# Performance work log

Hardware: AMD Instinct MI355X
Metric: run time of the kernel (lower is better)

The kernel has to match this reference:

```python
import jax, jax.numpy as jnp
import numpy as np

V, E, H, B, S = 32000, 1024, 1024, 64, 128


def setup_inputs() -> dict:
    key = jax.random.key(0)
    ks = jax.random.split(key, 16)
    s = 0.02
    return {
        "input_seq": jax.random.randint(ks[0], (B, 1), 0, V),
        "hidden": jax.random.normal(ks[1], (1, B, H), jnp.float32),
        "cell": jax.random.normal(ks[2], (1, B, H), jnp.float32),
        "encoder_outputs": jax.random.normal(ks[3], (B, S, H), jnp.float32),
        "emb": jax.random.normal(ks[4], (V, E), jnp.float32) * s,
        "Wa_w": jax.random.normal(ks[5], (H, H), jnp.float32) * s,
        "Wa_b": jnp.zeros((H,), jnp.float32),
        "Ua_w": jax.random.normal(ks[6], (H, H), jnp.float32) * s,
        "Ua_b": jnp.zeros((H,), jnp.float32),
        "Va_w": jax.random.normal(ks[7], (1, H), jnp.float32) * s,
        "Va_b": jnp.zeros((1,), jnp.float32),
        "W_ih": jax.random.normal(ks[8], (4 * H, E + H), jnp.float32) * s,
        "W_hh": jax.random.normal(ks[9], (4 * H, H), jnp.float32) * s,
        "b_ih": jnp.zeros((4 * H,), jnp.float32),
        "b_hh": jnp.zeros((4 * H,), jnp.float32),
        "out_w": jax.random.normal(ks[10], (V, H), jnp.float32) * s,
        "out_b": jnp.zeros((V,), jnp.float32),
    }


def reference(input_seq, hidden, cell, encoder_outputs, emb, Wa_w, Wa_b, Ua_w, Ua_b,
              Va_w, Va_b, W_ih, W_hh, b_ih, b_hh, out_w, out_b):
    # embedding lookup (dropout p=0 -> identity): [B,1,E]
    embedded = emb[input_seq]
    # query = last layer hidden: [B,1,H]
    query = hidden[-1][:, None, :]
    # Bahdanau additive attention
    q_proj = query @ Wa_w.T + Wa_b                       # [B,1,H]
    k_proj = encoder_outputs @ Ua_w.T + Ua_b             # [B,S,H]
    scores = jnp.tanh(q_proj + k_proj) @ Va_w.T + Va_b   # [B,S,1]
    scores = scores[..., 0][:, None, :]                  # [B,1,S]
    weights = jax.nn.softmax(scores, axis=-1)            # [B,1,S]
    context = jnp.einsum('bqs,bsh->bqh', weights, encoder_outputs)  # [B,1,H]
    # LSTM single step on concat(embedded, context)
    x = jnp.concatenate([embedded, context], axis=2)[:, 0, :]  # [B,E+H]
    h0, c0 = hidden[0], cell[0]
    gates = x @ W_ih.T + b_ih + h0 @ W_hh.T + b_hh       # [B,4H]
    i, f, g, o = jnp.split(gates, 4, axis=-1)
    c1 = jax.nn.sigmoid(f) * c0 + jax.nn.sigmoid(i) * jnp.tanh(g)
    h1 = jax.nn.sigmoid(o) * jnp.tanh(c1)
    output = h1[:, None, :]                              # [B,1,H]
    logits = output @ out_w.T + out_b                    # [B,1,V]
    return logits, h1[None], c1[None], weights
```

## Files before the change

### kernel.cpp

```cpp
#include <hip/hip_runtime.h>
#include <hip/hip_bf16.h>

using short8 = __attribute__((ext_vector_type(8))) short;
using f32x4  = __attribute__((ext_vector_type(4))) float;

__device__ inline unsigned pk2(float lo, float hi) {
    __hip_bfloat162 h = __float22bfloat162_rn(float2{lo, hi});
    return *reinterpret_cast<unsigned*>(&h);
}
__device__ inline short8 cvt8(float4 a, float4 b) {
    union { unsigned u[4]; short8 s; } r;
    r.u[0] = pk2(a.x, a.y); r.u[1] = pk2(a.z, a.w);
    r.u[2] = pk2(b.x, b.y); r.u[3] = pk2(b.z, b.w);
    return r.s;
}
__device__ inline float ftanh(float x) {
    float e = __expf(2.f * x);
    return 1.f - 2.f / (e + 1.f);
}
__device__ inline void gload16(const void* g, void* lds) {
    __builtin_amdgcn_global_load_lds(
        (const __attribute__((address_space(1))) unsigned int*)g,
        (__attribute__((address_space(3))) unsigned int*)lds, 16, 0, 0);
}
__device__ inline short f2b(float f) {
    unsigned u = __float_as_uint(f);
    return (short)((u + 0x7FFFu + ((u >> 16) & 1u)) >> 16);
}

__global__ void k_init(const int* __restrict__ idx, const float* __restrict__ emb,
                       const float* __restrict__ h0, float* __restrict__ xcat,
                       float4* __restrict__ wsz) {
    int i = blockIdx.x * blockDim.x + threadIdx.x;
    if (i < 18432) {
        float4 z = {0.f, 0.f, 0.f, 0.f};
        wsz[i] = z;
    } else if (i < 67584) {
        int j = i - 18432;
        int b = j / 768, q = j - b * 768;
        if (q < 256)
            ((float4*)(xcat + (size_t)b * 3072))[q] =
                ((const float4*)(emb + (size_t)idx[b] * 1024))[q];
        else if (q >= 512)
            ((float4*)(xcat + (size_t)b * 3072))[q] =
                ((const float4*)(h0 + (size_t)b * 1024))[q - 512];
    }
}

__global__ void k_cvt_swz(const float* __restrict__ enc, const float* __restrict__ Ua,
                          short* __restrict__ dst) {
    int i = blockIdx.x * blockDim.x + threadIdx.x;
    if (i >= 9216 * 128) return;
    int row = i >> 7, gi = i & 127;
    int seg = gi >> 3, g = gi & 7;
    const float* src = (row < 8192) ? enc + ((size_t)row << 10)
                                    : Ua + ((size_t)(row - 8192) << 10);
    const float* p = src + (seg << 6) + ((g ^ (row & 7)) << 3);
    float4 v0 = *(const float4*)p;
    float4 v1 = *(const float4*)(p + 4);
    *(short8*)&dst[(size_t)i << 3] = cvt8(v0, v1);
}

__global__ __launch_bounds__(512) void k_attn2(
    const short* __restrict__ Abf, const short* __restrict__ Bbf,
    const float* __restrict__ Uab, const float* __restrict__ Wab,
    const float* __restrict__ qp, const float* __restrict__ Va,
    float* __restrict__ scores) {
    __shared__ short As[2][256 * 64];
    __shared__ short Bs[2][128 * 64];
    const int t = threadIdx.x;
    const int l = t & 63, w = t >> 6;
    const int wm = w >> 1, wn = w & 1;
    const int lr = l & 15, lg = l >> 4;
    const int n0 = blockIdx.x * 128;
    const int r0 = blockIdx.y * 256;

    f32x4 acc[4][4];
#pragma unroll
    for (int i = 0; i < 4; ++i)
#pragma unroll
        for (int j = 0; j < 4; ++j) { f32x4 z = {0.f, 0.f, 0.f, 0.f}; acc[i][j] = z; }

    auto STAGE = [&](int buf, int seg) {
#pragma unroll
        for (int i = 0; i < 4; ++i) {
            int base = i * 512 + w * 64;
            int s = base + l;
            gload16(Abf + (((size_t)r0 + (s >> 3)) << 10) + (seg << 6) + ((s & 7) << 3),
                    (void*)&As[buf][base * 8]);
            if (i < 2)
                gload16(Bbf + (((size_t)8192 + n0 + (s >> 3)) << 10) + (seg << 6) + ((s & 7) << 3),
                        (void*)&Bs[buf][base * 8]);
        }
    };

    STAGE(0, 0);
    __syncthreads();

    for (int seg = 0; seg < 16; ++seg) {
        const int cur = seg & 1;
        if (seg < 15) STAGE(cur ^ 1, seg + 1);
#pragma unroll
        for (int kh = 0; kh < 2; ++kh) {
            short8 a[4], b[4];
#pragma unroll
            for (int i = 0; i < 4; ++i) {
                int ra = wm * 64 + i * 16 + lr;
                a[i] = *(const short8*)&As[cur][ra * 64 + (((kh * 4 + lg) ^ (ra & 7)) << 3)];
                int rb = wn * 64 + i * 16 + lr;
                b[i] = *(const short8*)&Bs[cur][rb * 64 + (((kh * 4 + lg) ^ (rb & 7)) << 3)];
            }
#pragma unroll
            for (int i = 0; i < 4; ++i)
#pragma unroll
                for (int j = 0; j < 4; ++j)
                    acc[i][j] = __builtin_amdgcn_mfma_f32_16x16x32_bf16(a[i], b[j], acc[i][j], 0, 0, 0);
        }
        __syncthreads();
    }

    float va[4], ub[4];
#pragma unroll
    for (int j = 0; j < 4; ++j) {
        int h = n0 + wn * 64 + j * 16 + lr;
        va[j] = Va[h];
        ub[j] = Uab[h] + Wab[h];
    }
#pragma unroll
    for (int i = 0; i < 4; ++i)
#pragma unroll
        for (int r = 0; r < 4; ++r) {
            int row = r0 + wm * 64 + i * 16 + lg * 4 + r;
            const float* qpb = qp + (size_t)(row >> 7) * 1024;
            float s = 0.f;
#pragma unroll
            for (int j = 0; j < 4; ++j) {
                int h = n0 + wn * 64 + j * 16 + lr;
                s += va[j] * ftanh(acc[i][j][r] + qpb[h] + ub[j]);
            }
            s += __shfl_xor(s, 1);
            s += __shfl_xor(s, 2);
            s += __shfl_xor(s, 4);
            s += __shfl_xor(s, 8);
            if (lr == 0) atomicAdd(scores + row, s);
        }
}

template <int EPI>
__global__ __launch_bounds__(256) void k_sgemm(
    const float* __restrict__ A, int lda,
    const float* __restrict__ B0, int ldb0,
    const float* __restrict__ B1, int ldb1, int kyB1,
    float* __restrict__ C, int ldc, int Kblk, int pstride) {
    __shared__ short As[64 * 64];
    __shared__ short Bs[64 * 64];
    const int t = threadIdx.x;
    const int l = t & 63, w = t >> 6;
    const int wm = w >> 1, wn = w & 1;
    const int lr = l & 15, lg = l >> 4;
    const int n0 = blockIdx.x * 64;
    const int ky = blockIdx.y;

    const float* Ab = A + (size_t)ky * Kblk;
    const float* Bb;
    int ldb;
    if (ky < kyB1) { Bb = B0 + (size_t)ky * Kblk; ldb = ldb0; }
    else           { Bb = B1 + (size_t)(ky - kyB1) * Kblk; ldb = ldb1; }

    f32x4 acc[2][2];
#pragma unroll
    for (int i = 0; i < 2; ++i)
#pragma unroll
        for (int j = 0; j < 2; ++j) { f32x4 z = {0.f, 0.f, 0.f, 0.f}; acc[i][j] = z; }

    for (int kt = 0; kt < Kblk; kt += 64) {
#pragma unroll
        for (int i = 0; i < 2; ++i) {
            int s = t + 256 * i, row = s >> 3, ch = s & 7;
            const float* p = Ab + (size_t)row * lda + kt + ch * 8;
            *(short8*)&As[row * 64 + ((ch ^ (row & 7)) << 3)] =
                cvt8(*(const float4*)p, *(const float4*)(p + 4));
            const float* q = Bb + (size_t)(n0 + row) * ldb + kt + ch * 8;
            *(short8*)&Bs[row * 64 + ((ch ^ (row & 7)) << 3)] =
                cvt8(*(const float4*)q, *(const float4*)(q + 4));
        }
        __syncthreads();
#pragma unroll
        for (int kh = 0; kh < 2; ++kh) {
            short8 a[2], b[2];
#pragma unroll
            for (int i = 0; i < 2; ++i) {
                int ra = wm * 32 + i * 16 + lr;
                a[i] = *(const short8*)&As[ra * 64 + (((kh * 4 + lg) ^ (ra & 7)) << 3)];
                int rb = wn * 32 + i * 16 + lr;
                b[i] = *(const short8*)&Bs[rb * 64 + (((kh * 4 + lg) ^ (rb & 7)) << 3)];
            }
#pragma unroll
            for (int i = 0; i < 2; ++i)
#pragma unroll
                for (int j = 0; j < 2; ++j)
                    acc[i][j] = __builtin_amdgcn_mfma_f32_16x16x32_bf16(a[i], b[j], acc[i][j], 0, 0, 0);
        }
        __syncthreads();
    }

    float* Cp = (EPI == 0) ? C + (size_t)ky * pstride : C;
#pragma unroll
    for (int i = 0; i < 2; ++i)
#pragma unroll
        for (int j = 0; j < 2; ++j)
#pragma unroll
            for (int r = 0; r < 4; ++r) {
                int R = wm * 32 + i * 16 + lg * 4 + r;
                int c = n0 + wn * 32 + j * 16 + lr;
                if constexpr (EPI == 1)
                    atomicAdd(&C[(size_t)R * ldc + c], acc[i][j][r]);
                else
                    Cp[(size_t)R * ldc + c] = acc[i][j][r];
            }
}

__global__ __launch_bounds__(256) void k_vgemm(
    const short* __restrict__ Abf, const float* __restrict__ B,
    const float* __restrict__ bias, float* __restrict__ C) {
    const int t = threadIdx.x;
    const int l = t & 63, w = t >> 6;
    const int lr = l & 15, lg = l >> 4;
    const int n0 = blockIdx.x * 64 + w * 16;

    f32x4 acc[4];
#pragma unroll
    for (int i = 0; i < 4; ++i) { f32x4 z = {0.f, 0.f, 0.f, 0.f}; acc[i] = z; }

    const float* bp = B + (size_t)(n0 + lr) * 1024 + lg * 8;
    const short* ap = Abf + lr * 1024 + lg * 8;

#pragma unroll 4
    for (int k0 = 0; k0 < 1024; k0 += 32) {
        float4 b0 = *(const float4*)(bp + k0);
        float4 b1 = *(const float4*)(bp + k0 + 4);
        short8 a0 = *(const short8*)(ap + k0);
        short8 a1 = *(const short8*)(ap + k0 + 16 * 1024);
        short8 a2 = *(const short8*)(ap + k0 + 32 * 1024);
        short8 a3 = *(const short8*)(ap + k0 + 48 * 1024);
        short8 bf = cvt8(b0, b1);
        acc[0] = __builtin_amdgcn_mfma_f32_16x16x32_bf16(a0, bf, acc[0], 0, 0, 0);
        acc[1] = __builtin_amdgcn_mfma_f32_16x16x32_bf16(a1, bf, acc[1], 0, 0, 0);
        acc[2] = __builtin_amdgcn_mfma_f32_16x16x32_bf16(a2, bf, acc[2], 0, 0, 0);
        acc[3] = __builtin_amdgcn_mfma_f32_16x16x32_bf16(a3, bf, acc[3], 0, 0, 0);
    }

    float bv = bias[n0 + lr];
#pragma unroll
    for (int i = 0; i < 4; ++i)
#pragma unroll
        for (int r = 0; r < 4; ++r)
            C[(size_t)(i * 16 + lg * 4 + r) * 32000 + n0 + lr] = acc[i][r] + bv;
}

__global__ __launch_bounds__(256) void k_smctx(
    const float* __restrict__ scores, const float* __restrict__ enc,
    float* __restrict__ wout, float* __restrict__ xcat) {
    int b = blockIdx.x;
    int t = threadIdx.x;
    __shared__ float buf[128];
    __shared__ float wsb[128];
    if (t < 128) buf[t] = scores[b * 128 + t];
    __syncthreads();
    if (t < 64) buf[t] = fmaxf(buf[t], buf[t + 64]);
    __syncthreads();
    if (t < 32) buf[t] = fmaxf(buf[t], buf[t + 32]);
    __syncthreads();
    float m;
    {
        float v = buf[t & 31];
        for (int off = 16; off > 0; off >>= 1)
            v = fmaxf(v, __shfl_xor(v, off, 32));
        m = v;
    }
    __syncthreads();
    if (t < 128) wsb[t] = __expf(scores[b * 128 + t] - m);
    __syncthreads();
    if (t < 64) buf[t] = wsb[t] + wsb[t + 64];
    __syncthreads();
    if (t < 32) buf[t] += buf[t + 32];
    __syncthreads();
    float sum;
    {
        float v = buf[t & 31];
        for (int off = 16; off > 0; off >>= 1)
            v += __shfl_xor(v, off, 32);
        sum = v;
    }
    float inv = 1.f / sum;
    __syncthreads();
    if (t < 128) {
        wsb[t] *= inv;
        wout[b * 128 + t] = wsb[t];
    }
    __syncthreads();
    float acc[4] = {0.f, 0.f, 0.f, 0.f};
    for (int s = 0; s < 128; ++s) {
        float wv = wsb[s];
        const float* row = enc + ((size_t)b * 128 + s) * 1024;
#pragma unroll
        for (int j = 0; j < 4; ++j) acc[j] += wv * row[t + 256 * j];
    }
#pragma unroll
    for (int j = 0; j < 4; ++j) xcat[(size_t)b * 3072 + 1024 + t + 256 * j] = acc[j];
}

__global__ void k_lstm6(const float* __restrict__ gp, const float* __restrict__ c0,
                        const float* __restrict__ b_ih, const float* __restrict__ b_hh,
                        float* __restrict__ h1, float* __restrict__ c1,
                        short* __restrict__ h1bf) {
    int idx = blockIdx.x * blockDim.x + threadIdx.x;
    int b = idx >> 10, h = idx & 1023;
    const float* g0 = gp + (size_t)b * 4096;
    float iv = b_ih[h] + b_hh[h];
    float fv = b_ih[1024 + h] + b_hh[1024 + h];
    float gv = b_ih[2048 + h] + b_hh[2048 + h];
    float ov = b_ih[3072 + h] + b_hh[3072 + h];
#pragma unroll
    for (int p = 0; p < 6; ++p) {
        const float* g = g0 + p * 262144;
        iv += g[h];
        fv += g[1024 + h];
        gv += g[2048 + h];
        ov += g[3072 + h];
    }
    float si = 1.f / (1.f + expf(-iv));
    float sf = 1.f / (1.f + expf(-fv));
    float so = 1.f / (1.f + expf(-ov));
    float tg = tanhf(gv);
    float cc = sf * c0[idx] + si * tg;
    float hh = so * tanhf(cc);
    c1[idx] = cc;
    h1[idx] = hh;
    h1bf[idx] = f2b(hh);
}

extern "C" void kernel_launch(void* const* d_in, const int* in_sizes, int n_in,
                              void* d_out, int out_size, void* d_ws, size_t ws_size,
                              hipStream_t stream) {
    const int* idx = (const int*)d_in[0];
    const float* hidden = (const float*)d_in[1];
    const float* cell = (const float*)d_in[2];
    const float* enc = (const float*)d_in[3];
    const float* emb = (const float*)d_in[4];
    const float* Wa_w = (const float*)d_in[5];
    const float* Wa_b = (const float*)d_in[6];
    const float* Ua_w = (const float*)d_in[7];
    const float* Ua_b = (const float*)d_in[8];
    const float* Va_w = (const float*)d_in[9];
    const float* W_ih = (const float*)d_in[11];
    const float* W_hh = (const float*)d_in[12];
    const float* b_ih = (const float*)d_in[13];
    const float* b_hh = (const float*)d_in[14];
    const float* out_w = (const float*)d_in[15];
    const float* out_b = (const float*)d_in[16];

    float* out = (float*)d_out;
    float* logits = out;
    float* h1 = out + 2048000;
    float* c1 = out + 2048000 + 65536;
    float* wts = out + 2048000 + 65536 + 65536;

    float* ws = (float*)d_ws;
    float* qp = ws;
    float* scores = ws + 65536;
    float* xcat = ws + 73728;
    float* gates_p = ws + 270336;
    short* h1_bf = (short*)(ws + 1843200);
    short* encua_bf = (short*)(ws + 1908736);

    k_init<<<264, 256, 0, stream>>>(idx, emb, hidden, xcat, (float4*)ws);
    k_cvt_swz<<<4608, 256, 0, stream>>>(enc, Ua_w, encua_bf);
    k_sgemm<1><<<dim3(16, 8), 256, 0, stream>>>(hidden, 1024, Wa_w, 1024,
                                                nullptr, 0, 99, qp, 1024, 128, 0);
    k_attn2<<<dim3(8, 32), 512, 0, stream>>>(encua_bf, encua_bf, Ua_b, Wa_b,
                                             qp, Va_w, scores);
    k_smctx<<<64, 256, 0, stream>>>(scores, enc, wts, xcat);
    k_sgemm<0><<<dim3(64, 6), 256, 0, stream>>>(xcat, 3072, W_ih, 2048,
                                                W_hh, 1024, 4, gates_p, 4096, 512, 262144);
    k_lstm6<<<256, 256, 0, stream>>>(gates_p, cell, b_ih, b_hh, h1, c1, h1_bf);
    k_vgemm<<<500, 256, 0, stream>>>(h1_bf, out_w, out_b, logits);
}
```

Before: 139.1 us.

## Merge prep kernels, reuse bf16 encoder copy for context, reorder attention grid

Combines the encoder/Ua bf16 conversion and the init kernel into a single launch. The softmax-context kernel now reads the swizzled bf16 encoder copy instead of the fp32 encoder, which halves its read traffic but adds bf16 rounding error to the context vector. The attention grid is transposed so that row blocks vary fastest, which changes the block scheduling order and likely improves L2 reuse of the B tile.

```diff
diff --git a/kernel.cpp b/kernel.cpp
--- a/kernel.cpp
+++ b/kernel.cpp
@@ -2,6 +2,7 @@
 #include <hip/hip_bf16.h>
 
 using short8 = __attribute__((ext_vector_type(8))) short;
+using short4v = __attribute__((ext_vector_type(4))) short;
 using f32x4  = __attribute__((ext_vector_type(4))) float;
 
 __device__ inline unsigned pk2(float lo, float hi) {
@@ -27,38 +28,40 @@
     unsigned u = __float_as_uint(f);
     return (short)((u + 0x7FFFu + ((u >> 16) & 1u)) >> 16);
 }
-
-__global__ void k_init(const int* __restrict__ idx, const float* __restrict__ emb,
+__device__ inline float b2f(short s) {
+    return __uint_as_float(((unsigned)(unsigned short)s) << 16);
+}
+
+__global__ void k_prep(const float* __restrict__ enc, const float* __restrict__ Ua,
+                       short* __restrict__ dst,
+                       const int* __restrict__ idx, const float* __restrict__ emb,
                        const float* __restrict__ h0, float* __restrict__ xcat,
                        float4* __restrict__ wsz) {
-    int i = blockIdx.x * blockDim.x + threadIdx.x;
-    if (i < 18432) {
-        float4 z = {0.f, 0.f, 0.f, 0.f};
-        wsz[i] = z;
-    } else if (i < 67584) {
-        int j = i - 18432;
-        int b = j / 768, q = j - b * 768;
-        if (q < 256)
-            ((float4*)(xcat + (size_t)b * 3072))[q] =
-                ((const float4*)(emb + (size_t)idx[b] * 1024))[q];
-        else if (q >= 512)
-            ((float4*)(xcat + (size_t)b * 3072))[q] =
-                ((const float4*)(h0 + (size_t)b * 1024))[q - 512];
-    }
-}
-
-__global__ void k_cvt_swz(const float* __restrict__ enc, const float* __restrict__ Ua,
-                          short* __restrict__ dst) {
-    int i = blockIdx.x * blockDim.x + threadIdx.x;
-    if (i >= 9216 * 128) return;
-    int row = i >> 7, gi = i & 127;
-    int seg = gi >> 3, g = gi & 7;
-    const float* src = (row < 8192) ? enc + ((size_t)row << 10)
-                                    : Ua + ((size_t)(row - 8192) << 10);
-    const float* p = src + (seg << 6) + ((g ^ (row & 7)) << 3);
-    float4 v0 = *(const float4*)p;
-    float4 v1 = *(const float4*)(p + 4);
-    *(short8*)&dst[(size_t)i << 3] = cvt8(v0, v1);
+    const int bid = blockIdx.x, t = threadIdx.x;
+    if (bid < 4608) {
+        int i = bid * 256 + t;
+        int row = i >> 7, gi = i & 127;
+        int seg = gi >> 3, g = gi & 7;
+        const float* src = (row < 8192) ? enc + ((size_t)row << 10)
+                                        : Ua + ((size_t)(row - 8192) << 10);
+        const float* p = src + (seg << 6) + ((g ^ (row & 7)) << 3);
+        *(short8*)&dst[(size_t)i << 3] = cvt8(*(const float4*)p, *(const float4*)(p + 4));
+    } else {
+        int i = (bid - 4608) * 256 + t;
+        if (i < 18432) {
+            float4 z = {0.f, 0.f, 0.f, 0.f};
+            wsz[i] = z;
+        } else if (i < 67584) {
+            int j = i - 18432;
+            int b = j / 768, q = j - b * 768;
+            if (q < 256)
+                ((float4*)(xcat + (size_t)b * 3072))[q] =
+                    ((const float4*)(emb + (size_t)idx[b] * 1024))[q];
+            else if (q >= 512)
+                ((float4*)(xcat + (size_t)b * 3072))[q] =
+                    ((const float4*)(h0 + (size_t)b * 1024))[q - 512];
+        }
+    }
 }
 
 __global__ __launch_bounds__(512) void k_attn2(
@@ -72,8 +75,8 @@
     const int l = t & 63, w = t >> 6;
     const int wm = w >> 1, wn = w & 1;
     const int lr = l & 15, lg = l >> 4;
-    const int n0 = blockIdx.x * 128;
-    const int r0 = blockIdx.y * 256;
+    const int r0 = blockIdx.x * 256;
+    const int n0 = blockIdx.y * 128;
 
     f32x4 acc[4][4];
 #pragma unroll
@@ -259,7 +262,7 @@
 }
 
 __global__ __launch_bounds__(256) void k_smctx(
-    const float* __restrict__ scores, const float* __restrict__ enc,
+    const float* __restrict__ scores, const short* __restrict__ enc_bf,
     float* __restrict__ wout, float* __restrict__ xcat) {
     int b = blockIdx.x;
     int t = threadIdx.x;
@@ -299,15 +302,21 @@
         wout[b * 128 + t] = wsb[t];
     }
     __syncthreads();
-    float acc[4] = {0.f, 0.f, 0.f, 0.f};
+    int h = t * 4;
+    int seg = h >> 6, g = (h >> 3) & 7, e0 = h & 7;
+    const short* basebf = enc_bf + (((size_t)b * 128) << 10) + (seg << 6) + e0;
+    float a0 = 0.f, a1 = 0.f, a2 = 0.f, a3 = 0.f;
     for (int s = 0; s < 128; ++s) {
         float wv = wsb[s];
-        const float* row = enc + ((size_t)b * 128 + s) * 1024;
-#pragma unroll
-        for (int j = 0; j < 4; ++j) acc[j] += wv * row[t + 256 * j];
-    }
-#pragma unroll
-    for (int j = 0; j < 4; ++j) xcat[(size_t)b * 3072 + 1024 + t + 256 * j] = acc[j];
+        const short* p = basebf + ((size_t)s << 10) + ((g ^ (s & 7)) << 3);
+        short4v v = *(const short4v*)p;
+        a0 += wv * b2f(v[0]);
+        a1 += wv * b2f(v[1]);
+        a2 += wv * b2f(v[2]);
+        a3 += wv * b2f(v[3]);
+    }
+    float4 o = {a0, a1, a2, a3};
+    *(float4*)&xcat[(size_t)b * 3072 + 1024 + h] = o;
 }
 
 __global__ void k_lstm6(const float* __restrict__ gp, const float* __restrict__ c0,
@@ -374,13 +383,13 @@
     short* h1_bf = (short*)(ws + 1843200);
     short* encua_bf = (short*)(ws + 1908736);
 
-    k_init<<<264, 256, 0, stream>>>(idx, emb, hidden, xcat, (float4*)ws);
-    k_cvt_swz<<<4608, 256, 0, stream>>>(enc, Ua_w, encua_bf);
+    k_prep<<<4872, 256, 0, stream>>>(enc, Ua_w, encua_bf, idx, emb, hidden,
+                                     xcat, (float4*)ws);
     k_sgemm<1><<<dim3(16, 8), 256, 0, stream>>>(hidden, 1024, Wa_w, 1024,
                                                 nullptr, 0, 99, qp, 1024, 128, 0);
-    k_attn2<<<dim3(8, 32), 512, 0, stream>>>(encua_bf, encua_bf, Ua_b, Wa_b,
+    k_attn2<<<dim3(32, 8), 512, 0, stream>>>(encua_bf, encua_bf, Ua_b, Wa_b,
                                              qp, Va_w, scores);
-    k_smctx<<<64, 256, 0, stream>>>(scores, enc, wts, xcat);
+    k_smctx<<<64, 256, 0, stream>>>(scores, encua_bf, wts, xcat);
     k_sgemm<0><<<dim3(64, 6), 256, 0, stream>>>(xcat, 3072, W_ih, 2048,
                                                 W_hh, 1024, 4, gates_p, 4096, 512, 262144);
     k_lstm6<<<256, 256, 0, stream>>>(gates_p, cell, b_ih, b_hh, h1, c1, h1_bf);
```

Measured after the change: 131.7 us (median of 3 runs). 1.06x faster.
